# Kernel optimization log

Hardware: AMD Instinct MI355X
Metric: run time of the kernel (lower is better)

The kernel has to match this reference:

```python
import jax, jax.numpy as jnp
import numpy as np

N_NODES = 100000
N_EDGES = 1600000
DIM = 128


def setup_inputs() -> dict:
    key = jax.random.key(0)
    k_x, k_e, k_wm, k_bm, k_wu, k_bu = jax.random.split(key, 6)
    bound = 1.0 / np.sqrt(DIM)
    return {
        "x": jax.random.normal(k_x, (N_NODES, DIM), dtype=jnp.float32),
        "edge_index": jax.random.randint(k_e, (2, N_EDGES), 0, N_NODES, dtype=jnp.int64),
        "W_msg": jax.random.uniform(k_wm, (DIM, DIM), jnp.float32, -bound, bound),
        "b_msg": jax.random.uniform(k_bm, (DIM,), jnp.float32, -bound, bound),
        "W_upd": jax.random.uniform(k_wu, (DIM, DIM), jnp.float32, -bound, bound),
        "b_upd": jax.random.uniform(k_bu, (DIM,), jnp.float32, -bound, bound),
    }


def reference(x, edge_index, W_msg, b_msg, W_upd, b_upd):
    # message_net: Linear + ReLU on all nodes  [N, D]
    messages = jax.nn.relu(x @ W_msg.T + b_msg)
    src, dst = edge_index[0], edge_index[1]
    # gather by src, scatter-add by dst (index_add)  [N, D]
    aggregated = jax.ops.segment_sum(messages[src], dst, num_segments=x.shape[0])
    # update_net: Linear + ReLU, then residual
    updated = jax.nn.relu(aggregated @ W_upd.T + b_upd)
    return updated + x
```

## Files before the change

### kernel.cpp

```cpp
#include <hip/hip_runtime.h>
#include <hip/hip_bf16.h>

#define DIM 128
#define BNODES 128
#define CNODES 1024
#define NCMAX 128
#define NBMAX 1024
#define CCAP 20480
#define BCAP 4096
#define SPLITB 8

typedef __attribute__((ext_vector_type(8))) short bf16x8;
typedef __attribute__((ext_vector_type(4))) float f32x4;

__device__ inline ushort f2bf(float f) {
    uint u = __float_as_uint(f);
    u += 0x7fffu + ((u >> 16) & 1u);
    return (ushort)(u >> 16);
}
__device__ inline uint pack2(float lo, float hi) {
    return (uint)f2bf(lo) | ((uint)f2bf(hi) << 16);
}

template<bool RESID, bool BF16OUT>
__global__ __launch_bounds__(256, 2)
void linear_mfma_kernel(const float* in, const float* __restrict__ W,
                        const float* __restrict__ b, const float* __restrict__ xres,
                        void* outv, int n_tiles)
{
    __shared__ uint4 Wl[128 * 16];

    const int t = threadIdx.x;
    for (int q = t; q < 2048; q += 256) {
        const int j = q >> 4, c = q & 15;
        const float4 lo = ((const float4*)(W + j * 128 + c * 8))[0];
        const float4 hi = ((const float4*)(W + j * 128 + c * 8))[1];
        uint4 pk;
        pk.x = pack2(lo.x, lo.y); pk.y = pack2(lo.z, lo.w);
        pk.z = pack2(hi.x, hi.y); pk.w = pack2(hi.z, hi.w);
        Wl[j * 16 + (c ^ (j & 15))] = pk;
    }
    __syncthreads();

    const int lane = t & 63;
    const int lo4 = lane & 15;
    const int g   = lane >> 4;

    float bias[8];
    #pragma unroll
    for (int ct = 0; ct < 8; ++ct) bias[ct] = b[ct * 16 + lo4];

    const int wid = (blockIdx.x * 256 + t) >> 6;
    const int nw  = (gridDim.x * 256) >> 6;

    for (int tile = wid; tile < n_tiles; tile += nw) {
        const int arow = tile * 16 + lo4;
        const float4* ap = (const float4*)(in + (size_t)arow * DIM + g * 32);
        float4 v[8];
        #pragma unroll
        for (int i = 0; i < 8; ++i) v[i] = ap[i];

        bf16x8 afrag[4];
        #pragma unroll
        for (int ks = 0; ks < 4; ++ks) {
            union { bf16x8 v8; uint u[4]; } a;
            a.u[0] = pack2(v[2*ks].x,   v[2*ks].y);
            a.u[1] = pack2(v[2*ks].z,   v[2*ks].w);
            a.u[2] = pack2(v[2*ks+1].x, v[2*ks+1].y);
            a.u[3] = pack2(v[2*ks+1].z, v[2*ks+1].w);
            afrag[ks] = a.v8;
        }

        f32x4 acc[8];
        #pragma unroll
        for (int ct = 0; ct < 8; ++ct)
            acc[ct] = (f32x4){bias[ct], bias[ct], bias[ct], bias[ct]};

        #pragma unroll
        for (int ks = 0; ks < 4; ++ks) {
            #pragma unroll
            for (int ct = 0; ct < 8; ++ct) {
                const int jrow = ct * 16 + lo4;
                const bf16x8 bfrag = *((const bf16x8*)&Wl[jrow * 16 + ((g * 4 + ks) ^ lo4)]);
                acc[ct] = __builtin_amdgcn_mfma_f32_16x16x32_bf16(afrag[ks], bfrag, acc[ct], 0, 0, 0);
            }
        }

        #pragma unroll
        for (int ct = 0; ct < 8; ++ct) {
            #pragma unroll
            for (int r = 0; r < 4; ++r) {
                const int orow = tile * 16 + g * 4 + r;
                const int ocol = ct * 16 + lo4;
                float val = fmaxf(acc[ct][r], 0.f);
                if constexpr (RESID) val += xres[(size_t)orow * DIM + ocol];
                if constexpr (BF16OUT)
                    ((ushort*)outv)[(size_t)orow * DIM + ocol] = f2bf(val);
                else
                    ((float*)outv)[(size_t)orow * DIM + ocol] = val;
            }
        }
    }
}

__global__ __launch_bounds__(256)
void coarse_scatter_kernel(const int* __restrict__ ei, int* __restrict__ ccur,
                           uint* __restrict__ cedges, int n_edges, int ncb)
{
    __shared__ int histL[NCMAX];
    __shared__ int curL[NCMAX];
    const int t = threadIdx.x;
    if (t < ncb) histL[t] = 0;
    __syncthreads();
    const int chunk = (n_edges + gridDim.x - 1) / gridDim.x;
    const int e0 = blockIdx.x * chunk;
    const int e1 = min(e0 + chunk, n_edges);
    for (int e = e0 + t; e < e1; e += 256)
        atomicAdd(&histL[ei[n_edges + e] >> 10], 1);
    __syncthreads();
    if (t < ncb)
        curL[t] = histL[t] ? atomicAdd(&ccur[t], histL[t]) : 0;
    __syncthreads();
    for (int e = e0 + t; e < e1; e += 256) {
        const int src = ei[e];
        const int dst = ei[n_edges + e];
        const int c = dst >> 10;
        const int pos = atomicAdd(&curL[c], 1);
        if (pos < CCAP)
            cedges[(size_t)c * CCAP + pos] = ((uint)src << 10) | (uint)(dst & 1023);
    }
}

__global__ __launch_bounds__(256)
void fine_scatter_kernel(const int* __restrict__ ccnt, const uint* __restrict__ cedges,
                         int* __restrict__ gcur, uint* __restrict__ bedges, int ncb)
{
    __shared__ int histL[SPLITB];
    __shared__ int curL[SPLITB];
    const int t = threadIdx.x;
    const int c = blockIdx.x / SPLITB;
    const int s = blockIdx.x % SPLITB;
    const int cnt = min(ccnt[c], CCAP);
    const int chunk = (cnt + SPLITB - 1) / SPLITB;
    const int e0 = s * chunk;
    const int e1 = min(e0 + chunk, cnt);
    if (t < SPLITB) histL[t] = 0;
    __syncthreads();
    const uint* ce = cedges + (size_t)c * CCAP;
    for (int i = e0 + t; i < e1; i += 256)
        atomicAdd(&histL[(ce[i] & 1023u) >> 7], 1);
    __syncthreads();
    if (t < SPLITB)
        curL[t] = histL[t] ? atomicAdd(&gcur[c * SPLITB + t], histL[t]) : 0;
    __syncthreads();
    for (int i = e0 + t; i < e1; i += 256) {
        const uint p = ce[i];
        const uint dl = p & 1023u;
        const int f = (int)(dl >> 7);
        const int pos = atomicAdd(&curL[f], 1);
        if (pos < BCAP)
            bedges[(size_t)(c * SPLITB + f) * BCAP + pos] = ((p >> 10) << 7) | (dl & 127u);
    }
}

__global__ __launch_bounds__(512)
void bucket_gather_kernel(const uint* __restrict__ msg, const int* __restrict__ gcur,
                          const uint* __restrict__ bedges, float* __restrict__ agg,
                          int n_nodes)
{
    __shared__ uint edgesL[BCAP];
    __shared__ int  srcL[BCAP];
    __shared__ int histL[BNODES];
    __shared__ int inclL[BNODES];
    __shared__ int cursL[BNODES];

    const int t = threadIdx.x;
    const int b = blockIdx.x;
    const int cnt = min(gcur[b], BCAP);
    const uint* be = bedges + (size_t)b * BCAP;

    if (t < BNODES) histL[t] = 0;
    __syncthreads();
    for (int i = t; i < cnt; i += 512) {
        const uint p = be[i];
        edgesL[i] = p;
        atomicAdd(&histL[p & 127u], 1);
    }
    __syncthreads();
    if (t < BNODES) inclL[t] = histL[t];
    for (int off = 1; off < BNODES; off <<= 1) {
        int add = 0;
        __syncthreads();
        if (t < BNODES && t >= off) add = inclL[t - off];
        __syncthreads();
        if (t < BNODES) inclL[t] += add;
    }
    __syncthreads();
    if (t < BNODES) cursL[t] = inclL[t] - histL[t];
    __syncthreads();
    for (int i = t; i < cnt; i += 512) {
        const uint p = edgesL[i];
        const int pos = atomicAdd(&cursL[p & 127u], 1);
        srcL[pos] = (int)(p >> 7);
    }
    __syncthreads();

    const int lane = t & 63;
    const int w = t >> 6;
    for (int dl = w; dl < BNODES; dl += 8) {
        const int node = b * BNODES + dl;
        if (node >= n_nodes) break;
        const int e1 = inclL[dl];
        const int e0 = e1 - histL[dl];
        float a0 = 0.f, a1 = 0.f;
        int i = e0;
        for (; i + 4 <= e1; i += 4) {
            const int sA = srcL[i + 0], sB = srcL[i + 1];
            const int sC = srcL[i + 2], sD = srcL[i + 3];
            const uint mA = msg[(size_t)sA * 64 + lane];
            const uint mB = msg[(size_t)sB * 64 + lane];
            const uint mC = msg[(size_t)sC * 64 + lane];
            const uint mD = msg[(size_t)sD * 64 + lane];
            a0 += __uint_as_float(mA << 16) + __uint_as_float(mB << 16)
                + __uint_as_float(mC << 16) + __uint_as_float(mD << 16);
            a1 += __uint_as_float(mA & 0xffff0000u) + __uint_as_float(mB & 0xffff0000u)
                + __uint_as_float(mC & 0xffff0000u) + __uint_as_float(mD & 0xffff0000u);
        }
        for (; i < e1; ++i) {
            const uint m = msg[(size_t)srcL[i] * 64 + lane];
            a0 += __uint_as_float(m << 16);
            a1 += __uint_as_float(m & 0xffff0000u);
        }
        ((float2*)(agg + (size_t)node * DIM))[lane] = make_float2(a0, a1);
    }
}

extern "C" void kernel_launch(void* const* d_in, const int* in_sizes, int n_in,
                              void* d_out, int out_size, void* d_ws, size_t ws_size,
                              hipStream_t stream)
{
    const float* x  = (const float*)d_in[0];
    const int*   ei = (const int*)d_in[1];
    const float* Wm = (const float*)d_in[2];
    const float* bm = (const float*)d_in[3];
    const float* Wu = (const float*)d_in[4];
    const float* bu = (const float*)d_in[5];

    const int N = in_sizes[0] / DIM;
    const int E = in_sizes[1] / 2;
    const int nb  = (N + BNODES - 1) / BNODES;
    const int ncb = (N + CNODES - 1) / CNODES;

    char* ws = (char*)d_ws;
    ushort* msg = (ushort*)ws;
    size_t o = (size_t)N * DIM * sizeof(ushort);
    int* ccur = (int*)(ws + o); o += (size_t)NCMAX * 4;
    int* gcur = (int*)(ws + o); o += (size_t)NBMAX * 4;
    o = (o + 255) & ~(size_t)255;
    uint* cedges = (uint*)(ws + o); o += (size_t)ncb * CCAP * 4;
    o = (o + 255) & ~(size_t)255;
    uint* bedges = (uint*)(ws + o);

    float* out = (float*)d_out;
    float* agg = out;

    const int n_tiles = N / 16;

    linear_mfma_kernel<false, true><<<1024, 256, 0, stream>>>(x, Wm, bm, nullptr, msg, n_tiles);

    hipMemsetAsync(ccur, 0, (size_t)(NCMAX + NBMAX) * 4, stream);
    coarse_scatter_kernel<<<1024, 256, 0, stream>>>(ei, ccur, cedges, E, ncb);
    fine_scatter_kernel<<<ncb * SPLITB, 256, 0, stream>>>(ccur, cedges, gcur, bedges, ncb);

    bucket_gather_kernel<<<nb, 512, 0, stream>>>((const uint*)msg, gcur, bedges, agg, N);

    linear_mfma_kernel<true, false><<<1024, 256, 0, stream>>>(agg, Wu, bu, x, out, n_tiles);
}
```

Baseline: 157.6 us.

## Fuse message linear with coarse edge scatter, halve gather bucket size

Result: no change. 157.7 us (+0.0%).

```diff
diff --git a/kernel.cpp b/kernel.cpp
--- a/kernel.cpp
+++ b/kernel.cpp
@@ -2,13 +2,13 @@
 #include <hip/hip_bf16.h>
 
 #define DIM 128
-#define BNODES 128
+#define BNODES 64
 #define CNODES 1024
 #define NCMAX 128
-#define NBMAX 1024
+#define NBMAX 2048
 #define CCAP 20480
-#define BCAP 4096
-#define SPLITB 8
+#define BCAP 2048
+#define FB 16
 
 typedef __attribute__((ext_vector_type(8))) short bf16x8;
 typedef __attribute__((ext_vector_type(4))) float f32x4;
@@ -23,13 +23,11 @@
 }
 
 template<bool RESID, bool BF16OUT>
-__global__ __launch_bounds__(256, 2)
-void linear_mfma_kernel(const float* in, const float* __restrict__ W,
-                        const float* __restrict__ b, const float* __restrict__ xres,
-                        void* outv, int n_tiles)
-{
-    __shared__ uint4 Wl[128 * 16];
-
+__device__ __forceinline__
+void linear_body(const float* in, const float* __restrict__ W,
+                 const float* __restrict__ b, const float* __restrict__ xres,
+                 void* outv, int n_tiles, int bid, int nblocks, uint4* Wl)
+{
     const int t = threadIdx.x;
     for (int q = t; q < 2048; q += 256) {
         const int j = q >> 4, c = q & 15;
@@ -50,8 +48,8 @@
     #pragma unroll
     for (int ct = 0; ct < 8; ++ct) bias[ct] = b[ct * 16 + lo4];
 
-    const int wid = (blockIdx.x * 256 + t) >> 6;
-    const int nw  = (gridDim.x * 256) >> 6;
+    const int wid = (bid * 256 + t) >> 6;
+    const int nw  = (nblocks * 256) >> 6;
 
     for (int tile = wid; tile < n_tiles; tile += nw) {
         const int arow = tile * 16 + lo4;
@@ -103,63 +101,82 @@
     }
 }
 
-__global__ __launch_bounds__(256)
-void coarse_scatter_kernel(const int* __restrict__ ei, int* __restrict__ ccur,
-                           uint* __restrict__ cedges, int n_edges, int ncb)
-{
+__global__ __launch_bounds__(256, 2)
+void lin1_coarse_kernel(const float* x, const float* __restrict__ Wm,
+                        const float* __restrict__ bm, ushort* msg, int n_tiles,
+                        const int* __restrict__ ei, int* __restrict__ ccur,
+                        uint* __restrict__ cedges, int n_edges, int ncb, int cblocks)
+{
+    __shared__ uint4 Wl[128 * 16];
     __shared__ int histL[NCMAX];
     __shared__ int curL[NCMAX];
-    const int t = threadIdx.x;
-    if (t < ncb) histL[t] = 0;
-    __syncthreads();
-    const int chunk = (n_edges + gridDim.x - 1) / gridDim.x;
-    const int e0 = blockIdx.x * chunk;
-    const int e1 = min(e0 + chunk, n_edges);
-    for (int e = e0 + t; e < e1; e += 256)
-        atomicAdd(&histL[ei[n_edges + e] >> 10], 1);
-    __syncthreads();
-    if (t < ncb)
-        curL[t] = histL[t] ? atomicAdd(&ccur[t], histL[t]) : 0;
-    __syncthreads();
-    for (int e = e0 + t; e < e1; e += 256) {
-        const int src = ei[e];
-        const int dst = ei[n_edges + e];
-        const int c = dst >> 10;
-        const int pos = atomicAdd(&curL[c], 1);
-        if (pos < CCAP)
-            cedges[(size_t)c * CCAP + pos] = ((uint)src << 10) | (uint)(dst & 1023);
-    }
+
+    if ((int)blockIdx.x < cblocks) {
+        const int t = threadIdx.x;
+        if (t < ncb) histL[t] = 0;
+        __syncthreads();
+        const int chunk = (n_edges + cblocks - 1) / cblocks;
+        const int e0 = blockIdx.x * chunk;
+        const int e1 = min(e0 + chunk, n_edges);
+        for (int e = e0 + t; e < e1; e += 256)
+            atomicAdd(&histL[ei[n_edges + e] >> 10], 1);
+        __syncthreads();
+        if (t < ncb)
+            curL[t] = histL[t] ? atomicAdd(&ccur[t], histL[t]) : 0;
+        __syncthreads();
+        for (int e = e0 + t; e < e1; e += 256) {
+            const int src = ei[e];
+            const int dst = ei[n_edges + e];
+            const int c = dst >> 10;
+            const int pos = atomicAdd(&curL[c], 1);
+            if (pos < CCAP)
+                cedges[(size_t)c * CCAP + pos] = ((uint)src << 10) | (uint)(dst & 1023);
+        }
+    } else {
+        linear_body<false, true>(x, Wm, bm, nullptr, msg, n_tiles,
+                                 (int)blockIdx.x - cblocks, (int)gridDim.x - cblocks, Wl);
+    }
+}
+
+__global__ __launch_bounds__(256, 2)
+void lin2_kernel(const float* agg, const float* __restrict__ Wu,
+                 const float* __restrict__ bu, const float* __restrict__ x,
+                 float* out, int n_tiles)
+{
+    __shared__ uint4 Wl[128 * 16];
+    linear_body<true, false>(agg, Wu, bu, x, out, n_tiles,
+                             (int)blockIdx.x, (int)gridDim.x, Wl);
 }
 
 __global__ __launch_bounds__(256)
 void fine_scatter_kernel(const int* __restrict__ ccnt, const uint* __restrict__ cedges,
                          int* __restrict__ gcur, uint* __restrict__ bedges, int ncb)
 {
-    __shared__ int histL[SPLITB];
-    __shared__ int curL[SPLITB];
+    __shared__ int histL[FB];
+    __shared__ int curL[FB];
     const int t = threadIdx.x;
-    const int c = blockIdx.x / SPLITB;
-    const int s = blockIdx.x % SPLITB;
+    const int c = blockIdx.x >> 3;
+    const int s = blockIdx.x & 7;
     const int cnt = min(ccnt[c], CCAP);
-    const int chunk = (cnt + SPLITB - 1) / SPLITB;
+    const int chunk = (cnt + 7) / 8;
     const int e0 = s * chunk;
     const int e1 = min(e0 + chunk, cnt);
-    if (t < SPLITB) histL[t] = 0;
+    if (t < FB) histL[t] = 0;
     __syncthreads();
     const uint* ce = cedges + (size_t)c * CCAP;
     for (int i = e0 + t; i < e1; i += 256)
-        atomicAdd(&histL[(ce[i] & 1023u) >> 7], 1);
-    __syncthreads();
-    if (t < SPLITB)
-        curL[t] = histL[t] ? atomicAdd(&gcur[c * SPLITB + t], histL[t]) : 0;
+        atomicAdd(&histL[(ce[i] & 1023u) >> 6], 1);
+    __syncthreads();
+    if (t < FB)
+        curL[t] = histL[t] ? atomicAdd(&gcur[c * FB + t], histL[t]) : 0;
     __syncthreads();
     for (int i = e0 + t; i < e1; i += 256) {
         const uint p = ce[i];
         const uint dl = p & 1023u;
-        const int f = (int)(dl >> 7);
+        const int f = (int)(dl >> 6);
         const int pos = atomicAdd(&curL[f], 1);
         if (pos < BCAP)
-            bedges[(size_t)(c * SPLITB + f) * BCAP + pos] = ((p >> 10) << 7) | (dl & 127u);
+            bedges[(size_t)(c * FB + f) * BCAP + pos] = ((p >> 10) << 6) | (dl & 63u);
     }
 }
 
@@ -184,7 +201,7 @@
     for (int i = t; i < cnt; i += 512) {
         const uint p = be[i];
         edgesL[i] = p;
-        atomicAdd(&histL[p & 127u], 1);
+        atomicAdd(&histL[p & 63u], 1);
     }
     __syncthreads();
     if (t < BNODES) inclL[t] = histL[t];
@@ -200,8 +217,8 @@
     __syncthreads();
     for (int i = t; i < cnt; i += 512) {
         const uint p = edgesL[i];
-        const int pos = atomicAdd(&cursL[p & 127u], 1);
-        srcL[pos] = (int)(p >> 7);
+        const int pos = atomicAdd(&cursL[p & 63u], 1);
+        srcL[pos] = (int)(p >> 6);
     }
     __syncthreads();
 
@@ -266,13 +283,14 @@
 
     const int n_tiles = N / 16;
 
-    linear_mfma_kernel<false, true><<<1024, 256, 0, stream>>>(x, Wm, bm, nullptr, msg, n_tiles);
-
     hipMemsetAsync(ccur, 0, (size_t)(NCMAX + NBMAX) * 4, stream);
-    coarse_scatter_kernel<<<1024, 256, 0, stream>>>(ei, ccur, cedges, E, ncb);
-    fine_scatter_kernel<<<ncb * SPLITB, 256, 0, stream>>>(ccur, cedges, gcur, bedges, ncb);
+
+    lin1_coarse_kernel<<<2048, 256, 0, stream>>>(x, Wm, bm, msg, n_tiles,
+                                                 ei, ccur, cedges, E, ncb, 1024);
+
+    fine_scatter_kernel<<<ncb * 8, 256, 0, stream>>>(ccur, cedges, gcur, bedges, ncb);
 
     bucket_gather_kernel<<<nb, 512, 0, stream>>>((const uint*)msg, gcur, bedges, agg, N);
 
-    linear_mfma_kernel<true, false><<<1024, 256, 0, stream>>>(agg, Wu, bu, x, out, n_tiles);
-}
+    lin2_kernel<<<1024, 256, 0, stream>>>(agg, Wu, bu, x, out, n_tiles);
+}
```
